# Kernel tuning notes

Measured on AMD Instinct MI355X. Metric: run time of the kernel, lower is better.

## Reference

```python
import jax, jax.numpy as jnp
import numpy as np

B, T, S, H = 8, 512, 512, 128


def setup_inputs() -> dict:
    key = jax.random.key(0)
    ks = jax.random.split(key, 8)
    query = jax.random.normal(ks[0], (B, T, H), dtype=jnp.float32)
    encoder_outputs = jax.random.normal(ks[1], (B, S, H), dtype=jnp.float32)
    src_lengths = jax.random.randint(ks[2], (B,), 1, S + 1)
    src_lengths = src_lengths.at[0].set(S)  # torch mask width == lengths.max() must equal S
    scale = 1.0 / np.sqrt(H)
    W_h = jax.random.normal(ks[3], (H, H), dtype=jnp.float32) * scale
    W_s = jax.random.normal(ks[4], (H, H), dtype=jnp.float32) * scale
    v = jax.random.normal(ks[5], (H,), dtype=jnp.float32) * scale
    W_out_w = jax.random.normal(ks[6], (H, 2 * H), dtype=jnp.float32) * (1.0 / np.sqrt(2 * H))
    W_out_b = jax.random.normal(ks[7], (H,), dtype=jnp.float32) * 0.01
    return {"query": query, "encoder_outputs": encoder_outputs,
            "src_lengths": src_lengths, "W_h": W_h, "W_s": W_s, "v": v,
            "W_out_w": W_out_w, "W_out_b": W_out_b}


def reference(query, encoder_outputs, src_lengths, W_h, W_s, v, W_out_w, W_out_b):
    # query: (B,T,H); encoder_outputs: (B,S,H)
    S_ = encoder_outputs.shape[1]
    WS = jnp.einsum('bth,oh->bto', query, W_s)            # (B,T,H)
    WH = jnp.einsum('bsh,oh->bso', encoder_outputs, W_h)  # (B,S,H)
    # additive scores: v^T tanh(W_s s_t + W_h h_i)  -> (B,T,S)
    scores = jnp.einsum('btsh,h->bts', jnp.tanh(WS[:, :, None, :] + WH[:, None, :, :]), v)
    mask = jnp.arange(S_) < src_lengths[:, None]          # (B,S)
    # faithful quirk: original zeroes (not -inf) masked scores before softmax
    scores = jnp.where(mask[:, None, :], scores, 0.0)
    attn = jax.nn.softmax(scores, axis=-1)                # (B,T,S)
    ct = jnp.einsum('bts,bsh->bth', attn, encoder_outputs)
    concat = jnp.concatenate([ct, query], axis=-1)        # (B,T,2H)
    return jnp.tanh(jnp.einsum('btc,oc->bto', concat, W_out_w) + W_out_b)
```

## Files before the change

### kernel.cpp

```cpp
#include <hip/hip_runtime.h>

#define NB 8
#define NT 512
#define NS 512
#define NH 128
#define C2LOG2E 2.8853900817779268f

__device__ __forceinline__ float fast_exp2(float x) { return __builtin_amdgcn_exp2f(x); }
__device__ __forceinline__ float fast_rcp(float x)  { return __builtin_amdgcn_rcpf(x); }
__device__ __forceinline__ float fast_tanh(float x) {
  float e = fast_exp2(x * C2LOG2E);
  return 1.0f - 2.0f * fast_rcp(e + 1.0f);
}

__device__ __forceinline__ float dot4(float4 a, float4 b) {
  return (a.x * b.x + a.y * b.y) + (a.z * b.z + a.w * b.w);
}

__device__ __forceinline__ float2 pair_acc2(float e0, float e1, float v0, float v1,
                                            float2 f0, float2 f1, float2 acc) {
  float2 P0, P1, num, den;
  P0.x = fmaf(e0, f0.x, 1.0f); P0.y = fmaf(e0, f0.y, 1.0f);
  P1.x = fmaf(e1, f1.x, 1.0f); P1.y = fmaf(e1, f1.y, 1.0f);
  num.x = fmaf(v0, P1.x, v1 * P0.x); num.y = fmaf(v0, P1.y, v1 * P0.y);
  den.x = P0.x * P1.x; den.y = P0.y * P1.y;
  acc.x = fmaf(num.x, fast_rcp(den.x), acc.x);
  acc.y = fmaf(num.y, fast_rcp(den.y), acc.y);
  return acc;
}

__global__ __launch_bounds__(256) void bah_proj_kernel(
    const float* __restrict__ query, const float* __restrict__ enc,
    const float* __restrict__ W_s, const float* __restrict__ W_h,
    const float* __restrict__ Wout,
    float* __restrict__ EWS, float* __restrict__ EWHT, float* __restrict__ WTP) {
  __shared__ __align__(16) float lds_w[64 * 132];
  __shared__ __align__(16) float lds_x[32 * 132];
  int blk = blockIdx.x;
  if (blk >= 512) {
    int g = (blk - 512) * 256 + threadIdx.x;
    int c = g >> 6, k4 = g & 63;
    float4 w = *(const float4*)(Wout + c * 256 + k4 * 4);
    *(float4*)(WTP + k4 * 512 + c * 4) = w;
    return;
  }
  const bool is_wh = blk >= 256;
  const float* in = is_wh ? enc : query;
  const float* W  = is_wh ? W_h : W_s;
  blk &= 255;
  const int rb = blk >> 1, ch = blk & 1;
  const int r0 = rb * 32, c0 = ch * 64;
  const int tid = threadIdx.x;
  for (int i = tid; i < 2048; i += 256) {
    int r = i >> 5, c4 = i & 31;
    *(float4*)(lds_w + r * 132 + c4 * 4) =
        *(const float4*)(W + (c0 + r) * 128 + c4 * 4);
  }
  for (int i = tid; i < 1024; i += 256) {
    int r = i >> 5, c4 = i & 31;
    *(float4*)(lds_x + r * 132 + c4 * 4) =
        *(const float4*)(in + (r0 + r) * NH + c4 * 4);
  }
  __syncthreads();
  const int cg = tid & 31;
  const int rg = tid >> 5;
  float acc[4][2] = {{0,0},{0,0},{0,0},{0,0}};
  for (int k4 = 0; k4 < 32; ++k4) {
    float4 xa[4], wb[2];
    #pragma unroll
    for (int i = 0; i < 4; ++i)
      xa[i] = *(const float4*)(lds_x + (rg * 4 + i) * 132 + k4 * 4);
    #pragma unroll
    for (int m = 0; m < 2; ++m)
      wb[m] = *(const float4*)(lds_w + (cg + 32 * m) * 132 + k4 * 4);
    #pragma unroll
    for (int i = 0; i < 4; ++i)
      #pragma unroll
      for (int m = 0; m < 2; ++m)
        acc[i][m] += dot4(xa[i], wb[m]);
  }
  if (!is_wh) {
    #pragma unroll
    for (int i = 0; i < 4; ++i)
      #pragma unroll
      for (int m = 0; m < 2; ++m)
        EWS[(r0 + rg * 4 + i) * NH + c0 + cg + 32 * m] =
            fast_exp2(C2LOG2E * acc[i][m]);
  } else {
    __syncthreads();
    #pragma unroll
    for (int i = 0; i < 4; ++i)
      #pragma unroll
      for (int m = 0; m < 2; ++m)
        lds_x[(cg + 32 * m) * 33 + rg * 4 + i] = fast_exp2(C2LOG2E * acc[i][m]);
    __syncthreads();
    const int b = r0 >> 9, sl0 = r0 & 511;
    const int s_lane = tid & 31, hr = tid >> 5;
    #pragma unroll
    for (int j = 0; j < 8; ++j)
      EWHT[b * NH * NS + (c0 + hr * 8 + j) * NS + sl0 + s_lane] =
          lds_x[(hr * 8 + j) * 33 + s_lane];
  }
}

__global__ __launch_bounds__(512, 4) void bah_mega_kernel(
    const float* __restrict__ EWS, const float* __restrict__ EWHT,
    const float* __restrict__ v, const float* __restrict__ enc,
    const float* __restrict__ query, const float* __restrict__ WTP,
    const float* __restrict__ bias, const int* __restrict__ src_len,
    float* __restrict__ out) {
  __shared__ __align__(16) float smem[15872];
  float* s_v   = smem;
  float* s_et  = smem + 128;
  float* s_aT  = smem + 1184;
  float* s_par = smem + 5280;
  float* s_sc  = smem + 9632;
  float* s_ctq = smem + 13760;
  float* s_red = smem + 15808;

  const int tid = threadIdx.x;
  const int bb = blockIdx.x >> 6;
  const int t0 = (blockIdx.x & 63) * 8;
  const int len = src_len[bb];

  if (tid < 32) *(float4*)(s_v + tid * 4) = *(const float4*)(v + tid * 4);
  if (tid < 256) {
    int r = tid >> 5, c4 = tid & 31;
    *(float4*)(s_et + r * 132 + c4 * 4) =
        *(const float4*)(EWS + (bb * NT + t0 + r) * NH + c4 * 4);
  }
  __syncthreads();

  const int tg = tid >> 8, sp = tid & 255;
  const int sbase = sp * 2;
  const int h0 = tg * 64;
  float2 acc2[8];
  #pragma unroll
  for (int i = 0; i < 8; ++i) { acc2[i].x = 0.f; acc2[i].y = 0.f; }
  const int wave_s0 = (sp & ~63) * 2;
  if (wave_s0 < len) {
    const float* fb = EWHT + bb * NH * NS + h0 * NS + sbase;
    for (int ho = 0; ho < 8; ++ho) {
      const float* fh = fb + ho * 8 * NS;
      float2 F0 = *(const float2*)(fh + 0 * NS);
      float2 F1 = *(const float2*)(fh + 1 * NS);
      float2 F2 = *(const float2*)(fh + 2 * NS);
      float2 F3 = *(const float2*)(fh + 3 * NS);
      float2 F4 = *(const float2*)(fh + 4 * NS);
      float2 F5 = *(const float2*)(fh + 5 * NS);
      float2 F6 = *(const float2*)(fh + 6 * NS);
      float2 F7 = *(const float2*)(fh + 7 * NS);
      float4 va = *(const float4*)(s_v + h0 + ho * 8);
      float4 vb = *(const float4*)(s_v + h0 + ho * 8 + 4);
      #pragma unroll
      for (int tt = 0; tt < 8; ++tt) {
        float4 e0 = *(const float4*)(s_et + tt * 132 + h0 + ho * 8);
        float4 e1 = *(const float4*)(s_et + tt * 132 + h0 + ho * 8 + 4);
        acc2[tt] = pair_acc2(e0.x, e0.y, va.x, va.y, F0, F1, acc2[tt]);
        acc2[tt] = pair_acc2(e0.z, e0.w, va.z, va.w, F2, F3, acc2[tt]);
        acc2[tt] = pair_acc2(e1.x, e1.y, vb.x, vb.y, F4, F5, acc2[tt]);
        acc2[tt] = pair_acc2(e1.z, e1.w, vb.z, vb.w, F6, F7, acc2[tt]);
      }
    }
  }
  if (tg == 1) {
    #pragma unroll
    for (int tt = 0; tt < 8; ++tt)
      *(float2*)(s_par + sp * 17 + tt * 2) = acc2[tt];
  }
  __syncthreads();
  if (tg == 0) {
    float V0 = 0.f;
    #pragma unroll
    for (int i = 0; i < 32; ++i) {
      float4 t4 = *(const float4*)(s_v + i * 4);
      V0 += (t4.x + t4.y) + (t4.z + t4.w);
    }
    #pragma unroll
    for (int tt = 0; tt < 8; ++tt) {
      float2 oth = *(const float2*)(s_par + sp * 17 + tt * 2);
      float sx = acc2[tt].x + oth.x;
      float sy = acc2[tt].y + oth.y;
      float2 r;
      r.x = (sbase + 0 < len) ? fmaf(-2.f, sx, V0) : 0.f;
      r.y = (sbase + 1 < len) ? fmaf(-2.f, sy, V0) : 0.f;
      *(float2*)(s_sc + tt * 516 + sbase) = r;
    }
  }
  __syncthreads();

  const int t = tid & 7;
  const int c = tid >> 3;
  const int wv = tid >> 6;
  float pv[8];
  float mx = -3.4e38f;
  #pragma unroll
  for (int k = 0; k < 8; ++k) {
    pv[k] = s_sc[t * 516 + c + 64 * k];
    mx = fmaxf(mx, pv[k]);
  }
  #pragma unroll
  for (int msk = 8; msk <= 32; msk <<= 1)
    mx = fmaxf(mx, __shfl_xor(mx, msk, 64));
  if ((tid & 63) < 8) s_red[wv * 8 + t] = mx;
  __syncthreads();
  #pragma unroll
  for (int j = 1; j < 8; ++j) mx = fmaxf(mx, s_red[j * 8 + t]);
  mx = fmaxf(mx, s_red[t]);
  __syncthreads();
  float sum = 0.f;
  #pragma unroll
  for (int k = 0; k < 8; ++k) {
    pv[k] = fast_exp2((pv[k] - mx) * 1.4426950408889634f);
    sum += pv[k];
  }
  #pragma unroll
  for (int msk = 8; msk <= 32; msk <<= 1)
    sum += __shfl_xor(sum, msk, 64);
  if ((tid & 63) < 8) s_red[wv * 8 + t] = sum;
  __syncthreads();
  sum = 0.f;
  #pragma unroll
  for (int j = 0; j < 8; ++j) sum += s_red[j * 8 + t];
  const float rd = fast_rcp(sum);
  #pragma unroll
  for (int k = 0; k < 8; ++k)
    s_aT[(c + 64 * k) * 8 + t] = pv[k] * rd;
  __syncthreads();

  const int hg = tid & 31, sg = tid >> 5;
  float4 a8[8] = {{0,0,0,0},{0,0,0,0},{0,0,0,0},{0,0,0,0},
                  {0,0,0,0},{0,0,0,0},{0,0,0,0},{0,0,0,0}};
  const float* eb = enc + bb * NS * NH + hg * 4;
  for (int k = 0; k < 32; ++k) {
    int s = sg * 32 + k;
    float4 e  = *(const float4*)(eb + s * NH);
    float4 w0 = *(const float4*)(s_aT + s * 8);
    float4 w1 = *(const float4*)(s_aT + s * 8 + 4);
    a8[0].x += w0.x*e.x; a8[0].y += w0.x*e.y; a8[0].z += w0.x*e.z; a8[0].w += w0.x*e.w;
    a8[1].x += w0.y*e.x; a8[1].y += w0.y*e.y; a8[1].z += w0.y*e.z; a8[1].w += w0.y*e.w;
    a8[2].x += w0.z*e.x; a8[2].y += w0.z*e.y; a8[2].z += w0.z*e.z; a8[2].w += w0.z*e.w;
    a8[3].x += w0.w*e.x; a8[3].y += w0.w*e.y; a8[3].z += w0.w*e.z; a8[3].w += w0.w*e.w;
    a8[4].x += w1.x*e.x; a8[4].y += w1.x*e.y; a8[4].z += w1.x*e.z; a8[4].w += w1.x*e.w;
    a8[5].x += w1.y*e.x; a8[5].y += w1.y*e.y; a8[5].z += w1.y*e.z; a8[5].w += w1.y*e.w;
    a8[6].x += w1.z*e.x; a8[6].y += w1.z*e.y; a8[6].z += w1.z*e.z; a8[6].w += w1.z*e.w;
    a8[7].x += w1.w*e.x; a8[7].y += w1.w*e.y; a8[7].z += w1.w*e.z; a8[7].w += w1.w*e.w;
  }
  #pragma unroll
  for (int i = 0; i < 8; ++i) {
    a8[i].x += __shfl_xor(a8[i].x, 32, 64);
    a8[i].y += __shfl_xor(a8[i].y, 32, 64);
    a8[i].z += __shfl_xor(a8[i].z, 32, 64);
    a8[i].w += __shfl_xor(a8[i].w, 32, 64);
  }
  float* lred = s_par;
  if ((tid & 63) < 32) {
    #pragma unroll
    for (int i = 0; i < 8; ++i)
      *(float4*)(lred + wv * 1024 + i * 128 + hg * 4) = a8[i];
  }
  __syncthreads();
  if (tid < 256) {
    int tt = tid >> 5, hh = tid & 31;
    float4 o = {0.f, 0.f, 0.f, 0.f};
    #pragma unroll
    for (int j = 0; j < 8; ++j) {
      float4 p = *(const float4*)(lred + j * 1024 + tt * 128 + hh * 4);
      o.x += p.x; o.y += p.y; o.z += p.z; o.w += p.w;
    }
    *(float4*)(s_ctq + tt * 128 + hh * 4) = o;
  } else {
    int r = tid - 256;
    int tt = r >> 5, hh = r & 31;
    *(float4*)(s_ctq + 1024 + tt * 128 + hh * 4) =
        *(const float4*)(query + (bb * NT + t0 + tt) * NH + hh * 4);
  }
  __syncthreads();

  const int cc = tid & 127, th = tid >> 7;
  const float* x0 = s_ctq + (th * 2) * 128;
  const float* x1 = x0 + 128;
  const float* y0 = s_ctq + 1024 + (th * 2) * 128;
  const float* y1 = y0 + 128;
  float a0 = 0.f, a1 = 0.f;
  for (int k4 = 0; k4 < 32; ++k4) {
    float4 w = *(const float4*)(WTP + k4 * 512 + cc * 4);
    a0 += dot4(*(const float4*)(x0 + k4 * 4), w);
    a1 += dot4(*(const float4*)(x1 + k4 * 4), w);
  }
  for (int k4 = 32; k4 < 64; ++k4) {
    float4 w = *(const float4*)(WTP + k4 * 512 + cc * 4);
    a0 += dot4(*(const float4*)(y0 + (k4 - 32) * 4), w);
    a1 += dot4(*(const float4*)(y1 + (k4 - 32) * 4), w);
  }
  const float bc = bias[cc];
  float* ob = out + (bb * NT + t0 + th * 2) * NH;
  ob[cc]      = fast_tanh(a0 + bc);
  ob[NH + cc] = fast_tanh(a1 + bc);
}

extern "C" void kernel_launch(void* const* d_in, const int* in_sizes, int n_in,
                              void* d_out, int out_size, void* d_ws, size_t ws_size,
                              hipStream_t stream) {
  const float* query = (const float*)d_in[0];
  const float* enc   = (const float*)d_in[1];
  const int*   slen  = (const int*)d_in[2];
  const float* W_h   = (const float*)d_in[3];
  const float* W_s   = (const float*)d_in[4];
  const float* v     = (const float*)d_in[5];
  const float* Woutw = (const float*)d_in[6];
  const float* Woutb = (const float*)d_in[7];
  float* out = (float*)d_out;

  float* ws = (float*)d_ws;
  float* EWS  = ws;
  float* EWHT = ws + 524288;
  float* WTP  = ws + 1048576;

  bah_proj_kernel<<<544, 256, 0, stream>>>(query, enc, W_s, W_h, Woutw,
                                           EWS, EWHT, WTP);
  bah_mega_kernel<<<512, 512, 0, stream>>>(EWS, EWHT, v, enc, query, WTP,
                                           Woutb, slen, out);
}
```

Before: 119.9 us.

## Precompute enc·Wout_ct and query·Wout_q projections, drop output GEMM from mega kernel

Uses linearity to move the output projection ahead of the attention: enc is multiplied by the ct half of W_out in the projection kernel, and query by the query half plus bias. The mega kernel then applies attention weights directly to the projected encoder rows and adds the precomputed query term before tanh, which removes the per-block output GEMM and its LDS staging. The projection kernel grows from 544 to 1024 blocks and writes two extra workspace arrays. The sum of v is now computed with a wave shuffle instead of a serial loop, and the launch-bounds occupancy hint and LDS size change.

Result: no change. 118.1 us (-1.6%).

```diff
diff --git a/kernel.cpp b/kernel.cpp
--- a/kernel.cpp
+++ b/kernel.cpp
@@ -32,29 +32,26 @@
 __global__ __launch_bounds__(256) void bah_proj_kernel(
     const float* __restrict__ query, const float* __restrict__ enc,
     const float* __restrict__ W_s, const float* __restrict__ W_h,
-    const float* __restrict__ Wout,
-    float* __restrict__ EWS, float* __restrict__ EWHT, float* __restrict__ WTP) {
+    const float* __restrict__ Wout, const float* __restrict__ Woutb,
+    float* __restrict__ EWS, float* __restrict__ EWHT,
+    float* __restrict__ ENCW, float* __restrict__ QW2) {
   __shared__ __align__(16) float lds_w[64 * 132];
   __shared__ __align__(16) float lds_x[32 * 132];
-  int blk = blockIdx.x;
-  if (blk >= 512) {
-    int g = (blk - 512) * 256 + threadIdx.x;
-    int c = g >> 6, k4 = g & 63;
-    float4 w = *(const float4*)(Wout + c * 256 + k4 * 4);
-    *(float4*)(WTP + k4 * 512 + c * 4) = w;
-    return;
-  }
-  const bool is_wh = blk >= 256;
-  const float* in = is_wh ? enc : query;
-  const float* W  = is_wh ? W_h : W_s;
-  blk &= 255;
+  const int set = blockIdx.x >> 8;
+  const int blk = blockIdx.x & 255;
   const int rb = blk >> 1, ch = blk & 1;
   const int r0 = rb * 32, c0 = ch * 64;
   const int tid = threadIdx.x;
+  const float* in = (set == 1 || set == 2) ? enc : query;
+  const float* Wb; int wst;
+  if (set == 0)      { Wb = W_s;        wst = 128; }
+  else if (set == 1) { Wb = W_h;        wst = 128; }
+  else if (set == 2) { Wb = Wout;       wst = 256; }
+  else               { Wb = Wout + 128; wst = 256; }
   for (int i = tid; i < 2048; i += 256) {
     int r = i >> 5, c4 = i & 31;
     *(float4*)(lds_w + r * 132 + c4 * 4) =
-        *(const float4*)(W + (c0 + r) * 128 + c4 * 4);
+        *(const float4*)(Wb + (c0 + r) * wst + c4 * 4);
   }
   for (int i = tid; i < 1024; i += 256) {
     int r = i >> 5, c4 = i & 31;
@@ -79,14 +76,14 @@
       for (int m = 0; m < 2; ++m)
         acc[i][m] += dot4(xa[i], wb[m]);
   }
-  if (!is_wh) {
+  if (set == 0) {
     #pragma unroll
     for (int i = 0; i < 4; ++i)
       #pragma unroll
       for (int m = 0; m < 2; ++m)
         EWS[(r0 + rg * 4 + i) * NH + c0 + cg + 32 * m] =
             fast_exp2(C2LOG2E * acc[i][m]);
-  } else {
+  } else if (set == 1) {
     __syncthreads();
     #pragma unroll
     for (int i = 0; i < 4; ++i)
@@ -100,23 +97,35 @@
     for (int j = 0; j < 8; ++j)
       EWHT[b * NH * NS + (c0 + hr * 8 + j) * NS + sl0 + s_lane] =
           lds_x[(hr * 8 + j) * 33 + s_lane];
-  }
-}
-
-__global__ __launch_bounds__(512, 4) void bah_mega_kernel(
+  } else if (set == 2) {
+    #pragma unroll
+    for (int i = 0; i < 4; ++i)
+      #pragma unroll
+      for (int m = 0; m < 2; ++m)
+        ENCW[(r0 + rg * 4 + i) * NH + c0 + cg + 32 * m] = acc[i][m];
+  } else {
+    #pragma unroll
+    for (int i = 0; i < 4; ++i)
+      #pragma unroll
+      for (int m = 0; m < 2; ++m) {
+        int c = c0 + cg + 32 * m;
+        QW2[(r0 + rg * 4 + i) * NH + c] = acc[i][m] + Woutb[c];
+      }
+  }
+}
+
+__global__ __launch_bounds__(512) void bah_mega_kernel(
     const float* __restrict__ EWS, const float* __restrict__ EWHT,
-    const float* __restrict__ v, const float* __restrict__ enc,
-    const float* __restrict__ query, const float* __restrict__ WTP,
-    const float* __restrict__ bias, const int* __restrict__ src_len,
+    const float* __restrict__ v, const float* __restrict__ ENCW,
+    const float* __restrict__ QW2, const int* __restrict__ src_len,
     float* __restrict__ out) {
-  __shared__ __align__(16) float smem[15872];
+  __shared__ __align__(16) float smem[13824];
   float* s_v   = smem;
   float* s_et  = smem + 128;
   float* s_aT  = smem + 1184;
   float* s_par = smem + 5280;
   float* s_sc  = smem + 9632;
-  float* s_ctq = smem + 13760;
-  float* s_red = smem + 15808;
+  float* s_red = smem + 13760;
 
   const int tid = threadIdx.x;
   const int bb = blockIdx.x >> 6;
@@ -130,6 +139,15 @@
         *(const float4*)(EWS + (bb * NT + t0 + r) * NH + c4 * 4);
   }
   __syncthreads();
+
+  float V0;
+  {
+    float2 vv = *(const float2*)(s_v + (tid & 63) * 2);
+    V0 = vv.x + vv.y;
+    #pragma unroll
+    for (int msk = 1; msk <= 32; msk <<= 1)
+      V0 += __shfl_xor(V0, msk, 64);
+  }
 
   const int tg = tid >> 8, sp = tid & 255;
   const int sbase = sp * 2;
@@ -170,12 +188,6 @@
   }
   __syncthreads();
   if (tg == 0) {
-    float V0 = 0.f;
-    #pragma unroll
-    for (int i = 0; i < 32; ++i) {
-      float4 t4 = *(const float4*)(s_v + i * 4);
-      V0 += (t4.x + t4.y) + (t4.z + t4.w);
-    }
     #pragma unroll
     for (int tt = 0; tt < 8; ++tt) {
       float2 oth = *(const float2*)(s_par + sp * 17 + tt * 2);
@@ -231,7 +243,7 @@
   const int hg = tid & 31, sg = tid >> 5;
   float4 a8[8] = {{0,0,0,0},{0,0,0,0},{0,0,0,0},{0,0,0,0},
                   {0,0,0,0},{0,0,0,0},{0,0,0,0},{0,0,0,0}};
-  const float* eb = enc + bb * NS * NH + hg * 4;
+  const float* eb = ENCW + bb * NS * NH + hg * 4;
   for (int k = 0; k < 32; ++k) {
     int s = sg * 32 + k;
     float4 e  = *(const float4*)(eb + s * NH);
@@ -268,35 +280,15 @@
       float4 p = *(const float4*)(lred + j * 1024 + tt * 128 + hh * 4);
       o.x += p.x; o.y += p.y; o.z += p.z; o.w += p.w;
     }
-    *(float4*)(s_ctq + tt * 128 + hh * 4) = o;
-  } else {
-    int r = tid - 256;
-    int tt = r >> 5, hh = r & 31;
-    *(float4*)(s_ctq + 1024 + tt * 128 + hh * 4) =
-        *(const float4*)(query + (bb * NT + t0 + tt) * NH + hh * 4);
-  }
-  __syncthreads();
-
-  const int cc = tid & 127, th = tid >> 7;
-  const float* x0 = s_ctq + (th * 2) * 128;
-  const float* x1 = x0 + 128;
-  const float* y0 = s_ctq + 1024 + (th * 2) * 128;
-  const float* y1 = y0 + 128;
-  float a0 = 0.f, a1 = 0.f;
-  for (int k4 = 0; k4 < 32; ++k4) {
-    float4 w = *(const float4*)(WTP + k4 * 512 + cc * 4);
-    a0 += dot4(*(const float4*)(x0 + k4 * 4), w);
-    a1 += dot4(*(const float4*)(x1 + k4 * 4), w);
-  }
-  for (int k4 = 32; k4 < 64; ++k4) {
-    float4 w = *(const float4*)(WTP + k4 * 512 + cc * 4);
-    a0 += dot4(*(const float4*)(y0 + (k4 - 32) * 4), w);
-    a1 += dot4(*(const float4*)(y1 + (k4 - 32) * 4), w);
-  }
-  const float bc = bias[cc];
-  float* ob = out + (bb * NT + t0 + th * 2) * NH;
-  ob[cc]      = fast_tanh(a0 + bc);
-  ob[NH + cc] = fast_tanh(a1 + bc);
+    const int row = bb * NT + t0 + tt;
+    float4 q4 = *(const float4*)(QW2 + row * NH + hh * 4);
+    float4 r;
+    r.x = fast_tanh(o.x + q4.x);
+    r.y = fast_tanh(o.y + q4.y);
+    r.z = fast_tanh(o.z + q4.z);
+    r.w = fast_tanh(o.w + q4.w);
+    *(float4*)(out + row * NH + hh * 4) = r;
+  }
 }
 
 extern "C" void kernel_launch(void* const* d_in, const int* in_sizes, int n_in,
@@ -315,10 +307,10 @@
   float* ws = (float*)d_ws;
   float* EWS  = ws;
   float* EWHT = ws + 524288;
-  float* WTP  = ws + 1048576;
-
-  bah_proj_kernel<<<544, 256, 0, stream>>>(query, enc, W_s, W_h, Woutw,
-                                           EWS, EWHT, WTP);
-  bah_mega_kernel<<<512, 512, 0, stream>>>(EWS, EWHT, v, enc, query, WTP,
-                                           Woutb, slen, out);
-}
+  float* ENCW = ws + 1048576;
+  float* QW2  = ws + 1572864;
+
+  bah_proj_kernel<<<1024, 256, 0, stream>>>(query, enc, W_s, W_h, Woutw,
+                                            Woutb, EWS, EWHT, ENCW, QW2);
+  bah_mega_kernel<<<512, 512, 0, stream>>>(EWS, EWHT, v, ENCW, QW2, slen, out);
+}
```
